# Kernel tuning notes

Measured on AMD Instinct MI355X. Metric: run time of the kernel, lower is better.

## Reference

```python
import jax, jax.numpy as jnp
from jax import lax
import numpy as np

IN_F, H1, OUT_F, P = 128, 64, 64, 0.25
B, T = 64, 2048


def setup_inputs() -> dict:
    key = jax.random.key(0)
    ks = jax.random.split(key, 12)
    def w(k, shape, fan_in):
        return jax.random.normal(k, shape, dtype=jnp.float32) / np.sqrt(fan_in).astype(np.float32)
    x = jax.random.normal(ks[0], (B, T, IN_F), dtype=jnp.float32)
    # PyTorch LSTM param layout: W_ih [4H, in], W_hh [4H, H], gate order i,f,g,o
    W_ih1 = w(ks[1], (4 * H1, IN_F), IN_F)
    W_hh1 = w(ks[2], (4 * H1, H1), H1)
    b_ih1 = jnp.zeros((4 * H1,), jnp.float32)
    b_hh1 = jnp.zeros((4 * H1,), jnp.float32)
    W_ih2 = w(ks[3], (4 * OUT_F, H1), H1)
    W_hh2 = w(ks[4], (4 * OUT_F, OUT_F), OUT_F)
    b_ih2 = jnp.zeros((4 * OUT_F,), jnp.float32)
    b_hh2 = jnp.zeros((4 * OUT_F,), jnp.float32)
    # Variational (locked) dropout masks: one per sequence, shared across timesteps,
    # inverted-dropout pre-scaled by 1/(1-p).
    keep = 1.0 - P
    mask1 = (jax.random.bernoulli(ks[5], keep, (B, H1)).astype(jnp.float32) / keep)
    mask2 = (jax.random.bernoulli(ks[6], keep, (B, OUT_F)).astype(jnp.float32) / keep)
    return {"x": x, "W_ih1": W_ih1, "W_hh1": W_hh1, "b_ih1": b_ih1, "b_hh1": b_hh1,
            "W_ih2": W_ih2, "W_hh2": W_hh2, "b_ih2": b_ih2, "b_hh2": b_hh2,
            "mask1": mask1, "mask2": mask2}


def _lstm(x, W_ih, W_hh, b_ih, b_hh):
    # x: [B,T,I]; returns all hidden states [B,T,H]
    Bd = x.shape[0]
    H = W_hh.shape[1]
    # Precompute input contribution for all timesteps (one big GEMM).
    xg = jnp.einsum('bti,gi->btg', x, W_ih) + b_ih + b_hh  # [B,T,4H]
    W_hh_T = W_hh.T  # [H,4H]
    def step(carry, xg_t):
        h, c = carry
        g = xg_t + h @ W_hh_T
        i, f, gg, o = jnp.split(g, 4, axis=-1)
        c = jax.nn.sigmoid(f) * c + jax.nn.sigmoid(i) * jnp.tanh(gg)
        h = jax.nn.sigmoid(o) * jnp.tanh(c)
        return (h, c), h
    h0 = jnp.zeros((Bd, H), x.dtype)
    c0 = jnp.zeros((Bd, H), x.dtype)
    _, hs = lax.scan(step, (h0, c0), jnp.swapaxes(xg, 0, 1))
    return jnp.swapaxes(hs, 0, 1)


def reference(x, W_ih1, W_hh1, b_ih1, b_hh1, W_ih2, W_hh2, b_ih2, b_hh2, mask1, mask2):
    out = _lstm(x, W_ih1, W_hh1, b_ih1, b_hh1) * mask1[:, None, :]
    out = _lstm(out, W_ih2, W_hh2, b_ih2, b_hh2) * mask2[:, None, :]
    return jax.nn.relu(out)
```

## Files before the change

kernel.cpp:

```cpp
#include <hip/hip_runtime.h>
#include <hip/hip_bf16.h>

#define BB 64
#define TT 2048
#define INF 128
#define HH 64
#define GG 256

__device__ __forceinline__ float sigm(float x) { return 1.0f / (1.0f + __expf(-x)); }
__device__ __forceinline__ float tanh_f(float x) {
  float e = __expf(2.0f * x);
  return 1.0f - 2.0f / (e + 1.0f);
}
__device__ __forceinline__ float bcast(float v, int l) {
  return __uint_as_float(__builtin_amdgcn_readlane(__float_as_uint(v), l));
}


#define XWL1(I)                                                   \
  { float4 a = Wp[t * 32 + (I)];                                  \
    w0[4*(I)] = a.x; w0[4*(I)+1] = a.y; w0[4*(I)+2] = a.z; w0[4*(I)+3] = a.w; \
    float4 b = Wp[(128 + t) * 32 + (I)];                          \
    w1[4*(I)] = b.x; w1[4*(I)+1] = b.y; w1[4*(I)+2] = b.z; w1[4*(I)+3] = b.w; }
#define XWL4(I) XWL1(I) XWL1((I)+1) XWL1((I)+2) XWL1((I)+3)
#define XWLOAD XWL4(0) XWL4(4) XWL4(8) XWL4(12) XWL4(16) XWL4(20) XWL4(24) XWL4(28)

#define XD1(L)                                                    \
  { float xa = bcast(curx, (L)); float xb = bcast(cury, (L));     \
    a0e = fmaf(xa, w0[2*(L)],   a0e); a0o = fmaf(xb, w0[2*(L)+1], a0o); \
    a1e = fmaf(xa, w1[2*(L)],   a1e); a1o = fmaf(xb, w1[2*(L)+1], a1o); }
#define XD8(L) XD1(L) XD1((L)+1) XD1((L)+2) XD1((L)+3) XD1((L)+4) XD1((L)+5) XD1((L)+6) XD1((L)+7)
#define XDOT64 XD8(0) XD8(8) XD8(16) XD8(24) XD8(32) XD8(40) XD8(48) XD8(56)

__global__ __launch_bounds__(128, 1) void xgemm(const float* __restrict__ X,
                                                const float* __restrict__ W,
                                                const float* __restrict__ bi,
                                                const float* __restrict__ bh,
                                                float* __restrict__ XG) {
  const int t = threadIdx.x;
  const int lane = t & 63;
  const long m0 = (long)blockIdx.x * 256;

  float w0[INF], w1[INF];
  const float4* Wp = (const float4*)W;
  XWLOAD
  const float bias0 = bi[t] + bh[t];
  const float bias1 = bi[128 + t] + bh[128 + t];

  const float2* Xp = (const float2*)X;
  float2 cur = Xp[(size_t)m0 * 64 + lane];
  float2 nx1 = Xp[(size_t)(m0 + 1) * 64 + lane];

  for (int mi = 0; mi < 256; ++mi) {
    const long m = m0 + mi;
    float2 nx2 = make_float2(0.f, 0.f);
    if (mi + 2 < 256) nx2 = Xp[(size_t)(m + 2) * 64 + lane];

    const float curx = cur.x, cury = cur.y;
    float a0e = bias0, a0o = 0.f, a1e = bias1, a1o = 0.f;
    XDOT64
    XG[(size_t)m * GG + t] = a0e + a0o;
    XG[(size_t)m * GG + 128 + t] = a1e + a1o;
    cur = nx1; nx1 = nx2;
  }
}

#define WL1(I)                                                                  \
  { float4 a = p[lane * 16 + (I)];                                              \
    wi[4*(I)] = a.x; wi[4*(I)+1] = a.y; wi[4*(I)+2] = a.z; wi[4*(I)+3] = a.w;   \
    float4 c = p[(64 + lane) * 16 + (I)];                                       \
    wf[4*(I)] = c.x; wf[4*(I)+1] = c.y; wf[4*(I)+2] = c.z; wf[4*(I)+3] = c.w;   \
    float4 d = p[(128 + lane) * 16 + (I)];                                      \
    wg[4*(I)] = d.x; wg[4*(I)+1] = d.y; wg[4*(I)+2] = d.z; wg[4*(I)+3] = d.w;   \
    float4 e = p[(192 + lane) * 16 + (I)];                                      \
    wo[4*(I)] = e.x; wo[4*(I)+1] = e.y; wo[4*(I)+2] = e.z; wo[4*(I)+3] = e.w; }
#define WL4(I) WL1(I) WL1((I)+1) WL1((I)+2) WL1((I)+3)
#define WLOAD WL4(0) WL4(4) WL4(8) WL4(12)

#define D1(K)                                              \
  { float hk = bcast(hv, (K));                             \
    ai = fmaf(hk, wi[(K)], ai); af = fmaf(hk, wf[(K)], af);\
    ag = fmaf(hk, wg[(K)], ag); ao = fmaf(hk, wo[(K)], ao); }
#define D8(K) D1(K) D1((K)+1) D1((K)+2) D1((K)+3) D1((K)+4) D1((K)+5) D1((K)+6) D1((K)+7)
#define DOT64 D8(0) D8(8) D8(16) D8(24) D8(32) D8(40) D8(48) D8(56)

__global__ __launch_bounds__(256, 1) void lstm2(const float* __restrict__ XG,
                                                const float* __restrict__ Whh1,
                                                const float* __restrict__ Wih2,
                                                const float* __restrict__ Whh2,
                                                const float* __restrict__ bi2,
                                                const float* __restrict__ bh2,
                                                const float* __restrict__ m1g,
                                                const float* __restrict__ m2g,
                                                float* __restrict__ out) {
  const int b = blockIdx.x;
  const int wid = threadIdx.x >> 6;
  const int lane = threadIdx.x & 63;

  __shared__ int f_w0, f_w1, f_w2;
  __shared__ __align__(16) float x2buf[4][HH];
  __shared__ __align__(16) float a2xbuf[4][GG];

  if (threadIdx.x == 0) { f_w0 = 0; f_w1 = 0; f_w2 = 0; }
  __syncthreads();
  if (wid == 3) return;

#define WAIT_GE(flag, tgt)                                   \
  do {                                                       \
    while (*(volatile int*)&(flag) < (tgt)) {}               \
    asm volatile("" ::: "memory");                           \
  } while (0)
#define PUBLISH(flag, val)                                   \
  do {                                                       \
    asm volatile("s_waitcnt lgkmcnt(0)" ::: "memory");       \
    if (lane == 0) *(volatile int*)&(flag) = (val);          \
  } while (0)

  if (wid == 0) {
    float wi[HH], wf[HH], wg[HH], wo[HH];
    const float4* p = (const float4*)Whh1;
    WLOAD
    const float m1 = m1g[b * HH + lane];
    const float* xgp = XG + (size_t)b * TT * GG;

    float cur0 = xgp[lane], cur1 = xgp[64 + lane], cur2 = xgp[128 + lane], cur3 = xgp[192 + lane];
    float n10 = xgp[GG + lane], n11 = xgp[GG + 64 + lane], n12 = xgp[GG + 128 + lane], n13 = xgp[GG + 192 + lane];

    float h1 = 0.f, c1 = 0.f;
    for (int s = 0; s < TT; ++s) {
      float n20 = 0.f, n21 = 0.f, n22 = 0.f, n23 = 0.f;
      if (s + 2 < TT) {
        const float* q = xgp + (size_t)(s + 2) * GG;
        n20 = q[lane]; n21 = q[64 + lane]; n22 = q[128 + lane]; n23 = q[192 + lane];
      }

      const float hv = h1;
      float ai = cur0, af = cur1, ag = cur2, ao = cur3;
      DOT64
      c1 = sigm(af) * c1 + sigm(ai) * tanh_f(ag);
      h1 = sigm(ao) * tanh_f(c1);

      WAIT_GE(f_w1, s - 3);
      x2buf[s & 3][lane] = h1 * m1;
      PUBLISH(f_w0, s + 1);

      cur0 = n10; cur1 = n11; cur2 = n12; cur3 = n13;
      n10 = n20; n11 = n21; n12 = n22; n13 = n23;
    }
  } else if (wid == 1) {
    float wi[HH], wf[HH], wg[HH], wo[HH];
    const float4* p = (const float4*)Wih2;
    WLOAD
    const float bi_i = bi2[lane] + bh2[lane];
    const float bi_f = bi2[64 + lane] + bh2[64 + lane];
    const float bi_g = bi2[128 + lane] + bh2[128 + lane];
    const float bi_o = bi2[192 + lane] + bh2[192 + lane];

    for (int s = 0; s < TT; ++s) {
      WAIT_GE(f_w0, s + 1);
      const float hv = x2buf[s & 3][lane];

      float ai = bi_i, af = bi_f, ag = bi_g, ao = bi_o;
      DOT64
      WAIT_GE(f_w2, s - 3);
      a2xbuf[s & 3][lane] = ai;
      a2xbuf[s & 3][64 + lane] = af;
      a2xbuf[s & 3][128 + lane] = ag;
      a2xbuf[s & 3][192 + lane] = ao;
      PUBLISH(f_w1, s + 1);
    }
  } else {
    float wi[HH], wf[HH], wg[HH], wo[HH];
    const float4* p = (const float4*)Whh2;
    WLOAD
    const float m2 = m2g[b * HH + lane];
    float* ob = out + (size_t)b * TT * HH;

    float h2 = 0.f, c2 = 0.f;
    for (int s = 0; s < TT; ++s) {
      const float hv = h2;
      float ai = 0.f, af = 0.f, ag = 0.f, ao = 0.f;
      DOT64

      WAIT_GE(f_w1, s + 1);
      ai += a2xbuf[s & 3][lane];
      af += a2xbuf[s & 3][64 + lane];
      ag += a2xbuf[s & 3][128 + lane];
      ao += a2xbuf[s & 3][192 + lane];

      c2 = sigm(af) * c2 + sigm(ai) * tanh_f(ag);
      h2 = sigm(ao) * tanh_f(c2);
      PUBLISH(f_w2, s + 1);
      ob[(size_t)s * HH + lane] = fmaxf(h2 * m2, 0.f);
    }
  }
#undef WAIT_GE
#undef PUBLISH
}

extern "C" void kernel_launch(void* const* d_in, const int* in_sizes, int n_in,
                              void* d_out, int out_size, void* d_ws, size_t ws_size,
                              hipStream_t stream) {
  (void)in_sizes; (void)n_in; (void)out_size; (void)ws_size;
  const float* x     = (const float*)d_in[0];
  const float* W_ih1 = (const float*)d_in[1];
  const float* W_hh1 = (const float*)d_in[2];
  const float* b_ih1 = (const float*)d_in[3];
  const float* b_hh1 = (const float*)d_in[4];
  const float* W_ih2 = (const float*)d_in[5];
  const float* W_hh2 = (const float*)d_in[6];
  const float* b_ih2 = (const float*)d_in[7];
  const float* b_hh2 = (const float*)d_in[8];
  const float* mask1 = (const float*)d_in[9];
  const float* mask2 = (const float*)d_in[10];
  float* out = (float*)d_out;

  float* xg1 = (float*)d_ws;

  xgemm<<<dim3(BB * TT / 256), dim3(128), 0, stream>>>(x, W_ih1, b_ih1, b_hh1, xg1);
  lstm2<<<dim3(BB), dim3(256), 0, stream>>>(xg1, W_hh1, W_ih2, W_hh2, b_ih2, b_hh2,
                                            mask1, mask2, out);
}
```

Baseline: 2.529 ms.

## Stage recurrent hidden state in LDS and tile input GEMM through shared memory

The recurrent dot products in the fused two-layer LSTM kernel now broadcast the hidden vector by reading it from LDS as float4, instead of issuing 64 per-step v_readlane broadcasts. This is meant to remove the serial readlane-to-SGPR hazards on the critical recurrence path, at the cost of an LDS write-then-read round trip each timestep. The input-projection GEMM is also restructured. It now uses 256 threads, each owning one gate row of weights in registers, and stages 64 rows of X at a time into shared memory for broadcast float4 reads. That replaces the previous lane-broadcast scheme, and the trade is shared-memory usage plus block barriers.

Result: slower. 3.120 ms (+23.4%).

```diff
diff --git a/kernel.cpp b/kernel.cpp
--- a/kernel.cpp
+++ b/kernel.cpp
@@ -12,56 +12,49 @@
   float e = __expf(2.0f * x);
   return 1.0f - 2.0f / (e + 1.0f);
 }
-__device__ __forceinline__ float bcast(float v, int l) {
-  return __uint_as_float(__builtin_amdgcn_readlane(__float_as_uint(v), l));
-}
-
-
-#define XWL1(I)                                                   \
-  { float4 a = Wp[t * 32 + (I)];                                  \
-    w0[4*(I)] = a.x; w0[4*(I)+1] = a.y; w0[4*(I)+2] = a.z; w0[4*(I)+3] = a.w; \
-    float4 b = Wp[(128 + t) * 32 + (I)];                          \
-    w1[4*(I)] = b.x; w1[4*(I)+1] = b.y; w1[4*(I)+2] = b.z; w1[4*(I)+3] = b.w; }
-#define XWL4(I) XWL1(I) XWL1((I)+1) XWL1((I)+2) XWL1((I)+3)
-#define XWLOAD XWL4(0) XWL4(4) XWL4(8) XWL4(12) XWL4(16) XWL4(20) XWL4(24) XWL4(28)
-
-#define XD1(L)                                                    \
-  { float xa = bcast(curx, (L)); float xb = bcast(cury, (L));     \
-    a0e = fmaf(xa, w0[2*(L)],   a0e); a0o = fmaf(xb, w0[2*(L)+1], a0o); \
-    a1e = fmaf(xa, w1[2*(L)],   a1e); a1o = fmaf(xb, w1[2*(L)+1], a1o); }
-#define XD8(L) XD1(L) XD1((L)+1) XD1((L)+2) XD1((L)+3) XD1((L)+4) XD1((L)+5) XD1((L)+6) XD1((L)+7)
-#define XDOT64 XD8(0) XD8(8) XD8(16) XD8(24) XD8(32) XD8(40) XD8(48) XD8(56)
-
-__global__ __launch_bounds__(128, 1) void xgemm(const float* __restrict__ X,
+
+#define XW1(I)                                                     \
+  { float4 a = Wp[(I)];                                            \
+    w[4*(I)] = a.x; w[4*(I)+1] = a.y; w[4*(I)+2] = a.z; w[4*(I)+3] = a.w; }
+#define XW4(I) XW1(I) XW1((I)+1) XW1((I)+2) XW1((I)+3)
+#define XWLOAD XW4(0) XW4(4) XW4(8) XW4(12) XW4(16) XW4(20) XW4(24) XW4(28)
+
+#define XF1(Ki)                                                    \
+  { float4 x4 = Xb[(Ki)];                                          \
+    a0 = fmaf(x4.x, w[4*(Ki)],   a0); a1 = fmaf(x4.y, w[4*(Ki)+1], a1); \
+    a2 = fmaf(x4.z, w[4*(Ki)+2], a2); a3 = fmaf(x4.w, w[4*(Ki)+3], a3); }
+#define XF4(Ki) XF1(Ki) XF1((Ki)+1) XF1((Ki)+2) XF1((Ki)+3)
+#define XF32 XF4(0) XF4(4) XF4(8) XF4(12) XF4(16) XF4(20) XF4(24) XF4(28)
+
+__global__ __launch_bounds__(256, 1) void xgemm(const float* __restrict__ X,
                                                 const float* __restrict__ W,
                                                 const float* __restrict__ bi,
                                                 const float* __restrict__ bh,
                                                 float* __restrict__ XG) {
+  __shared__ __align__(16) float Xs[64 * INF];
   const int t = threadIdx.x;
-  const int lane = t & 63;
   const long m0 = (long)blockIdx.x * 256;
 
-  float w0[INF], w1[INF];
-  const float4* Wp = (const float4*)W;
+  float w[INF];
+  const float4* Wp = (const float4*)(W + (size_t)t * INF);
   XWLOAD
-  const float bias0 = bi[t] + bh[t];
-  const float bias1 = bi[128 + t] + bh[128 + t];
-
-  const float2* Xp = (const float2*)X;
-  float2 cur = Xp[(size_t)m0 * 64 + lane];
-  float2 nx1 = Xp[(size_t)(m0 + 1) * 64 + lane];
-
-  for (int mi = 0; mi < 256; ++mi) {
-    const long m = m0 + mi;
-    float2 nx2 = make_float2(0.f, 0.f);
-    if (mi + 2 < 256) nx2 = Xp[(size_t)(m + 2) * 64 + lane];
-
-    const float curx = cur.x, cury = cur.y;
-    float a0e = bias0, a0o = 0.f, a1e = bias1, a1o = 0.f;
-    XDOT64
-    XG[(size_t)m * GG + t] = a0e + a0o;
-    XG[(size_t)m * GG + 128 + t] = a1e + a1o;
-    cur = nx1; nx1 = nx2;
+  const float bias = bi[t] + bh[t];
+
+  for (int tile = 0; tile < 4; ++tile) {
+    const float4* src = (const float4*)(X + (size_t)(m0 + tile * 64) * INF);
+#pragma unroll
+    for (int i = 0; i < 8; ++i) {
+      int idx = t + i * 256;
+      ((float4*)Xs)[idx] = src[idx];
+    }
+    __syncthreads();
+    for (int r = 0; r < 64; ++r) {
+      const float4* Xb = (const float4*)&Xs[r * INF];
+      float a0 = bias, a1 = 0.f, a2 = 0.f, a3 = 0.f;
+      XF32
+      XG[(size_t)(m0 + tile * 64 + r) * GG + t] = (a0 + a1) + (a2 + a3);
+    }
+    __syncthreads();
   }
 }
 
@@ -77,12 +70,19 @@
 #define WL4(I) WL1(I) WL1((I)+1) WL1((I)+2) WL1((I)+3)
 #define WLOAD WL4(0) WL4(4) WL4(8) WL4(12)
 
-#define D1(K)                                              \
-  { float hk = bcast(hv, (K));                             \
-    ai = fmaf(hk, wi[(K)], ai); af = fmaf(hk, wf[(K)], af);\
-    ag = fmaf(hk, wg[(K)], ag); ao = fmaf(hk, wo[(K)], ao); }
-#define D8(K) D1(K) D1((K)+1) D1((K)+2) D1((K)+3) D1((K)+4) D1((K)+5) D1((K)+6) D1((K)+7)
-#define DOT64 D8(0) D8(8) D8(16) D8(24) D8(32) D8(40) D8(48) D8(56)
+#define DL4(J, HB)                                                   \
+  { float4 h4 = (HB)[(J)];                                           \
+    ai = fmaf(h4.x, wi[4*(J)],   ai); af = fmaf(h4.x, wf[4*(J)],   af); \
+    ag = fmaf(h4.x, wg[4*(J)],   ag); ao = fmaf(h4.x, wo[4*(J)],   ao); \
+    ai = fmaf(h4.y, wi[4*(J)+1], ai); af = fmaf(h4.y, wf[4*(J)+1], af); \
+    ag = fmaf(h4.y, wg[4*(J)+1], ag); ao = fmaf(h4.y, wo[4*(J)+1], ao); \
+    ai = fmaf(h4.z, wi[4*(J)+2], ai); af = fmaf(h4.z, wf[4*(J)+2], af); \
+    ag = fmaf(h4.z, wg[4*(J)+2], ag); ao = fmaf(h4.z, wo[4*(J)+2], ao); \
+    ai = fmaf(h4.w, wi[4*(J)+3], ai); af = fmaf(h4.w, wf[4*(J)+3], af); \
+    ag = fmaf(h4.w, wg[4*(J)+3], ag); ao = fmaf(h4.w, wo[4*(J)+3], ao); }
+#define DOTL(HB) DL4(0,HB) DL4(1,HB) DL4(2,HB) DL4(3,HB) DL4(4,HB) DL4(5,HB) \
+                 DL4(6,HB) DL4(7,HB) DL4(8,HB) DL4(9,HB) DL4(10,HB) DL4(11,HB) \
+                 DL4(12,HB) DL4(13,HB) DL4(14,HB) DL4(15,HB)
 
 __global__ __launch_bounds__(256, 1) void lstm2(const float* __restrict__ XG,
                                                 const float* __restrict__ Whh1,
@@ -100,6 +100,8 @@
   __shared__ int f_w0, f_w1, f_w2;
   __shared__ __align__(16) float x2buf[4][HH];
   __shared__ __align__(16) float a2xbuf[4][GG];
+  __shared__ __align__(16) float h1loc[HH];
+  __shared__ __align__(16) float h2loc[HH];
 
   if (threadIdx.x == 0) { f_w0 = 0; f_w1 = 0; f_w2 = 0; }
   __syncthreads();
@@ -122,11 +124,12 @@
     WLOAD
     const float m1 = m1g[b * HH + lane];
     const float* xgp = XG + (size_t)b * TT * GG;
+    h1loc[lane] = 0.f;
 
     float cur0 = xgp[lane], cur1 = xgp[64 + lane], cur2 = xgp[128 + lane], cur3 = xgp[192 + lane];
     float n10 = xgp[GG + lane], n11 = xgp[GG + 64 + lane], n12 = xgp[GG + 128 + lane], n13 = xgp[GG + 192 + lane];
 
-    float h1 = 0.f, c1 = 0.f;
+    float c1 = 0.f;
     for (int s = 0; s < TT; ++s) {
       float n20 = 0.f, n21 = 0.f, n22 = 0.f, n23 = 0.f;
       if (s + 2 < TT) {
@@ -134,11 +137,12 @@
         n20 = q[lane]; n21 = q[64 + lane]; n22 = q[128 + lane]; n23 = q[192 + lane];
       }
 
-      const float hv = h1;
       float ai = cur0, af = cur1, ag = cur2, ao = cur3;
-      DOT64
+      const float4* Hb = (const float4*)h1loc;
+      DOTL(Hb)
       c1 = sigm(af) * c1 + sigm(ai) * tanh_f(ag);
-      h1 = sigm(ao) * tanh_f(c1);
+      float h1 = sigm(ao) * tanh_f(c1);
+      h1loc[lane] = h1;
 
       WAIT_GE(f_w1, s - 3);
       x2buf[s & 3][lane] = h1 * m1;
@@ -158,10 +162,10 @@
 
     for (int s = 0; s < TT; ++s) {
       WAIT_GE(f_w0, s + 1);
-      const float hv = x2buf[s & 3][lane];
+      const float4* Hb = (const float4*)x2buf[s & 3];
 
       float ai = bi_i, af = bi_f, ag = bi_g, ao = bi_o;
-      DOT64
+      DOTL(Hb)
       WAIT_GE(f_w2, s - 3);
       a2xbuf[s & 3][lane] = ai;
       a2xbuf[s & 3][64 + lane] = af;
@@ -175,12 +179,13 @@
     WLOAD
     const float m2 = m2g[b * HH + lane];
     float* ob = out + (size_t)b * TT * HH;
-
-    float h2 = 0.f, c2 = 0.f;
+    h2loc[lane] = 0.f;
+
+    float c2 = 0.f;
     for (int s = 0; s < TT; ++s) {
-      const float hv = h2;
       float ai = 0.f, af = 0.f, ag = 0.f, ao = 0.f;
-      DOT64
+      const float4* Hb = (const float4*)h2loc;
+      DOTL(Hb)
 
       WAIT_GE(f_w1, s + 1);
       ai += a2xbuf[s & 3][lane];
@@ -189,7 +194,8 @@
       ao += a2xbuf[s & 3][192 + lane];
 
       c2 = sigm(af) * c2 + sigm(ai) * tanh_f(ag);
-      h2 = sigm(ao) * tanh_f(c2);
+      float h2 = sigm(ao) * tanh_f(c2);
+      h2loc[lane] = h2;
       PUBLISH(f_w2, s + 1);
       ob[(size_t)s * HH + lane] = fmaxf(h2 * m2, 0.f);
     }
@@ -217,7 +223,7 @@
 
   float* xg1 = (float*)d_ws;
 
-  xgemm<<<dim3(BB * TT / 256), dim3(128), 0, stream>>>(x, W_ih1, b_ih1, b_hh1, xg1);
+  xgemm<<<dim3(BB * TT / 256), dim3(256), 0, stream>>>(x, W_ih1, b_ih1, b_hh1, xg1);
   lstm2<<<dim3(BB), dim3(256), 0, stream>>>(xg1, W_hh1, W_ih2, W_hh2, b_ih2, b_hh2,
                                             mask1, mask2, out);
 }
```
